# Kernel optimization log

Hardware: AMD Instinct MI355X
Metric: run time of the kernel (lower is better)

The kernel has to match this reference:

```python
import jax, jax.numpy as jnp
import numpy as np

B, L = 16384, 1024
BIAS = (1, 1)


def setup_inputs() -> dict:
    key = jax.random.key(0)
    k1, k2 = jax.random.split(key)
    c = jax.random.normal(k1, (B, L), dtype=jnp.float32)
    y = jax.random.randint(k2, (B, L), 0, 2, dtype=jnp.int32)
    return {"c": c, "y": y}


def reference(c, y):
    # BPMLL loss. The double sum over (k,l) in Y_i x Ybar_i of exp(c_l - c_k)
    # factors exactly: (sum_k y_k exp(-c_k)) * (sum_l ybar_l exp(c_l)).
    y_f = y.astype(jnp.float32)          # [B, L]
    y_bar = 1.0 - y_f                    # [B, L]
    y_norm = jnp.sum(y_f, axis=1) ** BIAS[0]        # [B]
    y_bar_norm = jnp.sum(y_bar, axis=1) ** BIAS[1]  # [B]
    pos_term = jnp.sum(y_f * jnp.exp(-c), axis=1)   # sum_k y_k exp(-c_k)
    neg_term = jnp.sum(y_bar * jnp.exp(c), axis=1)  # sum_l ybar_l exp(c_l)
    loss = (pos_term * neg_term) / (y_norm * y_bar_norm)  # [B]
    return jnp.mean(loss)  # reduction='mean' -> scalar
```

## Files before the change

kernel.cpp:

```cpp
#include <hip/hip_runtime.h>


#define NROWS 16384
#define NCOLS 1024
#define ROWS_PER_BLOCK 4
#define NBLOCKS (NROWS / ROWS_PER_BLOCK)

__global__ __launch_bounds__(256) void bpmll_rows_kernel(
    const float* __restrict__ c, const int* __restrict__ y,
    float* __restrict__ partials) {
    const int wave = threadIdx.x >> 6;
    const int lane = threadIdx.x & 63;
    const int row = blockIdx.x * ROWS_PER_BLOCK + wave;

    const float4* __restrict__ c4 = (const float4*)(c + (size_t)row * NCOLS);
    const int4* __restrict__ y4 = (const int4*)(y + (size_t)row * NCOLS);

    float pos = 0.f, neg = 0.f, ycnt = 0.f;
#pragma unroll
    for (int i = 0; i < NCOLS / (64 * 4); ++i) {
        float4 cv = c4[lane + 64 * i];
        int4 yv = y4[lane + 64 * i];
        {
            float t = __expf(yv.x ? -cv.x : cv.x);
            pos += yv.x ? t : 0.f;  neg += yv.x ? 0.f : t;  ycnt += (float)yv.x;
        }
        {
            float t = __expf(yv.y ? -cv.y : cv.y);
            pos += yv.y ? t : 0.f;  neg += yv.y ? 0.f : t;  ycnt += (float)yv.y;
        }
        {
            float t = __expf(yv.z ? -cv.z : cv.z);
            pos += yv.z ? t : 0.f;  neg += yv.z ? 0.f : t;  ycnt += (float)yv.z;
        }
        {
            float t = __expf(yv.w ? -cv.w : cv.w);
            pos += yv.w ? t : 0.f;  neg += yv.w ? 0.f : t;  ycnt += (float)yv.w;
        }
    }

#pragma unroll
    for (int off = 32; off > 0; off >>= 1) {
        pos += __shfl_down(pos, off);
        neg += __shfl_down(neg, off);
        ycnt += __shfl_down(ycnt, off);
    }

    __shared__ float acc[ROWS_PER_BLOCK];
    if (lane == 0) {
        const float yn = ycnt;
        const float ybn = (float)NCOLS - ycnt;
        acc[wave] = (pos * neg) / (yn * ybn);
    }
    __syncthreads();
    if (threadIdx.x == 0) {
        partials[blockIdx.x] =
            (acc[0] + acc[1] + acc[2] + acc[3]) * (1.0f / (float)NROWS);
    }
}

__global__ __launch_bounds__(1024) void bpmll_reduce_kernel(
    const float* __restrict__ partials, float* __restrict__ out) {
    float s = 0.f;
#pragma unroll
    for (int i = threadIdx.x; i < NBLOCKS; i += 1024) s += partials[i];
#pragma unroll
    for (int off = 32; off > 0; off >>= 1) s += __shfl_down(s, off);

    __shared__ float smem[16];
    const int lane = threadIdx.x & 63;
    const int wave = threadIdx.x >> 6;
    if (lane == 0) smem[wave] = s;
    __syncthreads();
    if (threadIdx.x == 0) {
        float t = 0.f;
#pragma unroll
        for (int w = 0; w < 16; ++w) t += smem[w];
        out[0] = t;
    }
}

extern "C" void kernel_launch(void* const* d_in, const int* in_sizes, int n_in,
                              void* d_out, int out_size, void* d_ws, size_t ws_size,
                              hipStream_t stream) {
    const float* c = (const float*)d_in[0];
    const int* y = (const int*)d_in[1];
    float* partials = (float*)d_ws;
    float* out = (float*)d_out;

    bpmll_rows_kernel<<<NBLOCKS, 256, 0, stream>>>(c, y, partials);
    bpmll_reduce_kernel<<<1, 1024, 0, stream>>>(partials, out);
}
```

Baseline: 142.4 us.

## Process multiple rows per wave with batched loads and fewer blocks

The row kernel now launches 1024 blocks, and each wave loops over four rows, handling two at a time. All float4/int4 loads for the pair are issued up front to raise memory-level parallelism. Per-row sums are reduced with xor shuffles and summed per wave, and the final reduce kernel shrinks to 256 threads with one float4 load each. This cuts block scheduling overhead and the partials count, but it lowers the total number of waves in flight and raises register pressure.

```diff
diff --git a/kernel.cpp b/kernel.cpp
--- a/kernel.cpp
+++ b/kernel.cpp
@@ -3,55 +3,77 @@
 
 #define NROWS 16384
 #define NCOLS 1024
-#define ROWS_PER_BLOCK 4
-#define NBLOCKS (NROWS / ROWS_PER_BLOCK)
+#define WPB 4
+#define NBLOCKS 1024
+#define ROWS_PER_WAVE (NROWS / (NBLOCKS * WPB))
 
-__global__ __launch_bounds__(256) void bpmll_rows_kernel(
+__device__ __forceinline__ void elem(float cv, int yv,
+                                     float& pos, float& neg, float& cnt) {
+    float t = __expf(yv ? -cv : cv);
+    pos += yv ? t : 0.f;
+    neg += yv ? 0.f : t;
+    cnt += (float)yv;
+}
+
+__global__ __launch_bounds__(256, 4) void bpmll_rows_kernel(
     const float* __restrict__ c, const int* __restrict__ y,
     float* __restrict__ partials) {
     const int wave = threadIdx.x >> 6;
     const int lane = threadIdx.x & 63;
-    const int row = blockIdx.x * ROWS_PER_BLOCK + wave;
+    const int gw = blockIdx.x * WPB + wave;
+    const int row0 = gw * ROWS_PER_WAVE;
 
-    const float4* __restrict__ c4 = (const float4*)(c + (size_t)row * NCOLS);
-    const int4* __restrict__ y4 = (const int4*)(y + (size_t)row * NCOLS);
+    float wave_loss = 0.f;
 
-    float pos = 0.f, neg = 0.f, ycnt = 0.f;
 #pragma unroll
-    for (int i = 0; i < NCOLS / (64 * 4); ++i) {
-        float4 cv = c4[lane + 64 * i];
-        int4 yv = y4[lane + 64 * i];
-        {
-            float t = __expf(yv.x ? -cv.x : cv.x);
-            pos += yv.x ? t : 0.f;  neg += yv.x ? 0.f : t;  ycnt += (float)yv.x;
+    for (int it = 0; it < ROWS_PER_WAVE / 2; ++it) {
+        const int rA = row0 + 2 * it;
+        const int rB = rA + 1;
+        const float4* __restrict__ cA = (const float4*)(c + (size_t)rA * NCOLS);
+        const float4* __restrict__ cB = (const float4*)(c + (size_t)rB * NCOLS);
+        const int4* __restrict__ yA = (const int4*)(y + (size_t)rA * NCOLS);
+        const int4* __restrict__ yB = (const int4*)(y + (size_t)rB * NCOLS);
+
+        float4 ca[4], cb[4];
+        int4 ya[4], yb[4];
+#pragma unroll
+        for (int i = 0; i < 4; ++i) ca[i] = cA[lane + 64 * i];
+#pragma unroll
+        for (int i = 0; i < 4; ++i) cb[i] = cB[lane + 64 * i];
+#pragma unroll
+        for (int i = 0; i < 4; ++i) ya[i] = yA[lane + 64 * i];
+#pragma unroll
+        for (int i = 0; i < 4; ++i) yb[i] = yB[lane + 64 * i];
+
+        float posA = 0.f, negA = 0.f, cntA = 0.f;
+        float posB = 0.f, negB = 0.f, cntB = 0.f;
+#pragma unroll
+        for (int i = 0; i < 4; ++i) {
+            elem(ca[i].x, ya[i].x, posA, negA, cntA);
+            elem(ca[i].y, ya[i].y, posA, negA, cntA);
+            elem(ca[i].z, ya[i].z, posA, negA, cntA);
+            elem(ca[i].w, ya[i].w, posA, negA, cntA);
+            elem(cb[i].x, yb[i].x, posB, negB, cntB);
+            elem(cb[i].y, yb[i].y, posB, negB, cntB);
+            elem(cb[i].z, yb[i].z, posB, negB, cntB);
+            elem(cb[i].w, yb[i].w, posB, negB, cntB);
         }
-        {
-            float t = __expf(yv.y ? -cv.y : cv.y);
-            pos += yv.y ? t : 0.f;  neg += yv.y ? 0.f : t;  ycnt += (float)yv.y;
+
+#pragma unroll
+        for (int off = 1; off < 64; off <<= 1) {
+            posA += __shfl_xor(posA, off);
+            negA += __shfl_xor(negA, off);
+            cntA += __shfl_xor(cntA, off);
+            posB += __shfl_xor(posB, off);
+            negB += __shfl_xor(negB, off);
+            cntB += __shfl_xor(cntB, off);
         }
-        {
-            float t = __expf(yv.z ? -cv.z : cv.z);
-            pos += yv.z ? t : 0.f;  neg += yv.z ? 0.f : t;  ycnt += (float)yv.z;
-        }
-        {
-            float t = __expf(yv.w ? -cv.w : cv.w);
-            pos += yv.w ? t : 0.f;  neg += yv.w ? 0.f : t;  ycnt += (float)yv.w;
-        }
+        wave_loss += (posA * negA) / (cntA * ((float)NCOLS - cntA))
+                   + (posB * negB) / (cntB * ((float)NCOLS - cntB));
     }
 
-#pragma unroll
-    for (int off = 32; off > 0; off >>= 1) {
-        pos += __shfl_down(pos, off);
-        neg += __shfl_down(neg, off);
-        ycnt += __shfl_down(ycnt, off);
-    }
-
-    __shared__ float acc[ROWS_PER_BLOCK];
-    if (lane == 0) {
-        const float yn = ycnt;
-        const float ybn = (float)NCOLS - ycnt;
-        acc[wave] = (pos * neg) / (yn * ybn);
-    }
+    __shared__ float acc[WPB];
+    if (lane == 0) acc[wave] = wave_loss;
     __syncthreads();
     if (threadIdx.x == 0) {
         partials[blockIdx.x] =
@@ -59,25 +81,19 @@
     }
 }
 
-__global__ __launch_bounds__(1024) void bpmll_reduce_kernel(
+__global__ __launch_bounds__(256) void bpmll_reduce_kernel(
     const float* __restrict__ partials, float* __restrict__ out) {
-    float s = 0.f;
+    float4 v = ((const float4*)partials)[threadIdx.x];
+    float s = v.x + v.y + v.z + v.w;
 #pragma unroll
-    for (int i = threadIdx.x; i < NBLOCKS; i += 1024) s += partials[i];
-#pragma unroll
-    for (int off = 32; off > 0; off >>= 1) s += __shfl_down(s, off);
+    for (int off = 1; off < 64; off <<= 1) s += __shfl_xor(s, off);
 
-    __shared__ float smem[16];
+    __shared__ float smem[4];
     const int lane = threadIdx.x & 63;
     const int wave = threadIdx.x >> 6;
     if (lane == 0) smem[wave] = s;
     __syncthreads();
-    if (threadIdx.x == 0) {
-        float t = 0.f;
-#pragma unroll
-        for (int w = 0; w < 16; ++w) t += smem[w];
-        out[0] = t;
-    }
+    if (threadIdx.x == 0) out[0] = smem[0] + smem[1] + smem[2] + smem[3];
 }
 
 extern "C" void kernel_launch(void* const* d_in, const int* in_sizes, int n_in,
@@ -89,5 +105,5 @@
     float* out = (float*)d_out;
 
     bpmll_rows_kernel<<<NBLOCKS, 256, 0, stream>>>(c, y, partials);
-    bpmll_reduce_kernel<<<1, 1024, 0, stream>>>(partials, out);
+    bpmll_reduce_kernel<<<1, 256, 0, stream>>>(partials, out);
 }
```

Result: no change. 141.4 us (-0.7%).
